# Optimization experiments

Measured on AMD Instinct MI355X. Metric: run time of the kernel, lower is better.

The kernel has to match this reference:

```python
import jax, jax.numpy as jnp
import numpy as np

THRESHOLD = 0.3
NEG_BIG = -2.0 ** 32  # matches tf -2**32 causal mask constant


def setup_inputs() -> dict:
    key = jax.random.key(0)
    kq, kt, kv = jax.random.split(key, 3)
    B, S, D = 16, 2048, 128
    Q = jax.random.normal(kq, (B, S, D), dtype=jnp.float32)
    T = jax.random.normal(kt, (B, S, D), dtype=jnp.float32)
    V = jax.random.normal(kv, (B, S, D), dtype=jnp.float32)
    return {"Q": Q, "T": T, "V": V}


def reference(Q, T, V):
    # scores: [B, S, S]
    A = jnp.einsum('bqd,bkd->bqk', Q, T)
    # Faithful to tf.where(A>thr, A, -2**32 * cast(A>thr)):
    # the false branch evaluates to 0 (mask is 0 there), NOT -2**32.
    A = jnp.where(A > THRESHOLD, A, jnp.zeros((), A.dtype))
    S = Q.shape[1]
    causal = jnp.triu(jnp.ones((S, S), dtype=bool), k=1)  # strictly upper = masked
    A = A + jnp.where(causal, jnp.asarray(NEG_BIG, A.dtype), jnp.zeros((), A.dtype))
    d_k = jnp.asarray(Q.shape[-1], A.dtype)
    A = A / jnp.sqrt(d_k)
    y = jax.nn.softmax(A, axis=-1)
    return jnp.einsum('bqk,bkd->bqd', y, V)
```

## Files before the change

### kernel.cpp

```cpp
#include <hip/hip_runtime.h>
#include <hip/hip_bf16.h>


#define S_LEN 2048
#define D_DIM 128
#define BQ 64
#define BK 64
#define THRESH 0.3f
#define SCALE 0.08838834764831845f

typedef __bf16 bf16x8 __attribute__((ext_vector_type(8)));
typedef float f32x4 __attribute__((ext_vector_type(4)));

__global__ void vt_kernel(const float* __restrict__ V, __bf16* __restrict__ Vt) {
    __shared__ float tile[64][65];
    int bid = blockIdx.x;
    int b  = bid >> 6;
    int t2 = bid & 63;
    int s0 = (t2 >> 1) * 64;
    int d0 = (t2 & 1) * 64;
    int tid = threadIdx.x;
    #pragma unroll
    for (int it = 0; it < 2; ++it) {
        int row = it * 32 + (tid >> 3);
        int c   = (tid & 7) * 8;
        const float* p = V + ((size_t)b * S_LEN + s0 + row) * D_DIM + d0 + c;
        *(f32x4*)(&tile[row][c])     = *(const f32x4*)p;
        *(f32x4*)(&tile[row][c + 4]) = *(const f32x4*)(p + 4);
    }
    __syncthreads();
    #pragma unroll
    for (int it = 0; it < 2; ++it) {
        int dr = it * 32 + (tid >> 3);
        int c  = (tid & 7) * 8;
        bf16x8 w;
        #pragma unroll
        for (int j = 0; j < 8; ++j) w[j] = (__bf16)tile[c + j][dr];
        *(bf16x8*)(Vt + ((size_t)b * D_DIM + d0 + dr) * S_LEN + s0 + c) = w;
    }
}

__global__ __launch_bounds__(512, 2)
void fa_kernel(const float* __restrict__ Q, const float* __restrict__ T,
               const __bf16* __restrict__ Vt, float* __restrict__ O) {
    __shared__ __align__(16) unsigned char smem[81920];

    const int bid = blockIdx.x;
    const int b   = bid & 15;
    const int pi  = bid >> 4;
    const int qtH = 31 - pi;
    const int L   = pi + 1;

    const int tid   = threadIdx.x;
    const int g     = tid >> 8;
    const int tid_g = tid & 255;
    const int lane  = tid & 63;
    const int wg    = tid >> 6;
    const int wv    = wg & 3;
    const int col   = lane & 15;
    const int quad  = lane >> 4;

    unsigned char* Tt = smem + g * 16384;
    unsigned char* Vl = smem + 32768 + g * 16384;
    unsigned char* Pw = smem + 65536 + wg * 2048;

    bf16x8 qf[4];
    auto loadQ = [&](int qt) {
        const float* qptr = Q + ((size_t)b * S_LEN + qt * BQ + wv * 16 + col) * D_DIM + quad * 8;
        #pragma unroll
        for (int kk = 0; kk < 4; ++kk) {
            f32x4 a = *(const f32x4*)(qptr + kk * 32);
            f32x4 c = *(const f32x4*)(qptr + kk * 32 + 4);
            #pragma unroll
            for (int j = 0; j < 4; ++j) { qf[kk][j] = (__bf16)a[j]; qf[kk][4 + j] = (__bf16)c[j]; }
        }
    };

    f32x4 oacc[8];
    float lsum[4];
    auto resetAcc = [&]() {
        #pragma unroll
        for (int dt = 0; dt < 8; ++dt) oacc[dt] = {0.f, 0.f, 0.f, 0.f};
        #pragma unroll
        for (int r = 0; r < 4; ++r) lsum[r] = 0.f;
    };

    f32x4 tr[8]; bf16x8 vr[4];
    auto loadTiles = [&](int k0) {
        #pragma unroll
        for (int it = 0; it < 4; ++it) {
            int flat = it * 2048 + tid_g * 8;
            int row = flat >> 7, c = flat & 127;
            const float* p = T + ((size_t)b * S_LEN + k0 + row) * D_DIM + c;
            tr[2 * it]     = *(const f32x4*)p;
            tr[2 * it + 1] = *(const f32x4*)(p + 4);
        }
        #pragma unroll
        for (int it = 0; it < 4; ++it) {
            int flat = it * 2048 + tid_g * 8;
            int d = flat >> 6, kk2 = flat & 63;
            vr[it] = *(const bf16x8*)(Vt + ((size_t)b * D_DIM + d) * S_LEN + k0 + kk2);
        }
    };
    auto storeTiles = [&]() {
        #pragma unroll
        for (int it = 0; it < 4; ++it) {
            int flat = it * 2048 + tid_g * 8;
            int row = flat >> 7, c = flat & 127;
            bf16x8 w;
            #pragma unroll
            for (int j = 0; j < 4; ++j) {
                w[j]     = (__bf16)tr[2 * it][j];
                w[4 + j] = (__bf16)tr[2 * it + 1][j];
            }
            *(bf16x8*)(Tt + row * 256 + ((c * 2) ^ ((row & 7) << 4))) = w;
        }
        #pragma unroll
        for (int it = 0; it < 4; ++it) {
            int flat = it * 2048 + tid_g * 8;
            int d = flat >> 6, kk2 = flat & 63;
            *(bf16x8*)(Vl + d * 128 + ((kk2 * 2) ^ ((d & 7) << 4))) = vr[it];
        }
    };

    auto computeTile = [&](bool diag) {
        f32x4 sacc[4];
        #pragma unroll
        for (int t = 0; t < 4; ++t) {
            sacc[t] = {0.f, 0.f, 0.f, 0.f};
            #pragma unroll
            for (int kk = 0; kk < 4; ++kk) {
                int row = t * 16 + col;
                bf16x8 bf = *(const bf16x8*)(Tt + row * 256 + ((kk * 64 + quad * 16) ^ ((row & 7) << 4)));
                sacc[t] = __builtin_amdgcn_mfma_f32_16x16x32_bf16(qf[kk], bf, sacc[t], 0, 0, 0);
            }
        }
        float p[4][4];
        #pragma unroll
        for (int t = 0; t < 4; ++t)
            #pragma unroll
            for (int r = 0; r < 4; ++r) {
                float s = sacc[t][r];
                float e = __expf(s * SCALE);
                float w = (s > THRESH) ? e : 1.0f;
                if (diag && (t * 16 + col > wv * 16 + quad * 4 + r)) w = 0.0f;
                p[t][r] = w;
            }
        #pragma unroll
        for (int r = 0; r < 4; ++r)
            lsum[r] += (p[0][r] + p[1][r]) + (p[2][r] + p[3][r]);

        #pragma unroll
        for (int t = 0; t < 4; ++t)
            #pragma unroll
            for (int r = 0; r < 4; ++r) {
                int row = quad * 4 + r;
                *(__bf16*)(Pw + row * 128 + (((t * 16 + col) * 2) ^ ((row & 7) << 4))) = (__bf16)p[t][r];
            }
        asm volatile("s_waitcnt lgkmcnt(0)" ::: "memory");

        #pragma unroll
        for (int ks = 0; ks < 2; ++ks) {
            bf16x8 af = *(const bf16x8*)(Pw + col * 128 + ((ks * 64 + quad * 16) ^ ((col & 7) << 4)));
            #pragma unroll
            for (int dt = 0; dt < 8; ++dt) {
                int row = dt * 16 + col;
                bf16x8 bf = *(const bf16x8*)(Vl + row * 128 + ((ks * 64 + quad * 16) ^ ((row & 7) << 4)));
                oacc[dt] = __builtin_amdgcn_mfma_f32_16x16x32_bf16(af, bf, oacc[dt], 0, 0, 0);
            }
        }
    };

    auto slotKT = [&](int s) -> int {
        if (s >= 17) return -1;
        if (g == 0) return s;
        if (s < L)  return s;
        if (s == L) return -1;
        return s + 15 - pi;
    };

    resetAcc();
    int qtile = (g == 0) ? qtH : pi;
    loadQ(qtile);

    loadTiles(0);
    storeTiles();
    __syncthreads();

    for (int s = 0; s < 17; ++s) {
        int kt  = slotKT(s);
        int ktn = slotKT(s + 1);
        if (ktn >= 0) loadTiles(ktn * BK);
        if (kt >= 0) {
            computeTile(kt == qtile);
        } else {
            float inv[4];
            #pragma unroll
            for (int r = 0; r < 4; ++r) {
                float l = lsum[r];
                l += __shfl_xor(l, 1); l += __shfl_xor(l, 2);
                l += __shfl_xor(l, 4); l += __shfl_xor(l, 8);
                inv[r] = 1.0f / l;
            }
            float* optr = O + ((size_t)b * S_LEN + (size_t)pi * BQ + wv * 16) * D_DIM;
            #pragma unroll
            for (int dt = 0; dt < 8; ++dt)
                #pragma unroll
                for (int r = 0; r < 4; ++r)
                    optr[(quad * 4 + r) * D_DIM + dt * 16 + col] = oacc[dt][r] * inv[r];
            resetAcc();
            qtile = qtH;
            loadQ(qtH);
        }
        __syncthreads();
        if (ktn >= 0) storeTiles();
        __syncthreads();
    }

    float lred[4];
    #pragma unroll
    for (int r = 0; r < 4; ++r) {
        float l = lsum[r];
        l += __shfl_xor(l, 1); l += __shfl_xor(l, 2);
        l += __shfl_xor(l, 4); l += __shfl_xor(l, 8);
        lred[r] = l;
    }

    if (g == 1) {
        #pragma unroll
        for (int dt = 0; dt < 8; ++dt)
            #pragma unroll
            for (int r = 0; r < 4; ++r) {
                int row = wv * 16 + quad * 4 + r;
                *(float*)(smem + row * 512 + (((dt * 16 + col) * 4) ^ ((row & 7) << 4))) = oacc[dt][r];
            }
        if (col == 0) {
            #pragma unroll
            for (int r = 0; r < 4; ++r)
                *(float*)(smem + 65536 + (wv * 16 + quad * 4 + r) * 4) = lred[r];
        }
    }
    __syncthreads();
    if (g == 0) {
        float inv[4];
        #pragma unroll
        for (int r = 0; r < 4; ++r) {
            int row = wv * 16 + quad * 4 + r;
            float lp = *(const float*)(smem + 65536 + row * 4);
            inv[r] = 1.0f / (lred[r] + lp);
        }
        float* optr = O + ((size_t)b * S_LEN + (size_t)qtH * BQ + wv * 16) * D_DIM;
        #pragma unroll
        for (int dt = 0; dt < 8; ++dt)
            #pragma unroll
            for (int r = 0; r < 4; ++r) {
                int row = wv * 16 + quad * 4 + r;
                float part = *(const float*)(smem + row * 512 + (((dt * 16 + col) * 4) ^ ((row & 7) << 4)));
                optr[(quad * 4 + r) * D_DIM + dt * 16 + col] = (oacc[dt][r] + part) * inv[r];
            }
    }
}

extern "C" void kernel_launch(void* const* d_in, const int* in_sizes, int n_in,
                              void* d_out, int out_size, void* d_ws, size_t ws_size,
                              hipStream_t stream) {
    const float* Q = (const float*)d_in[0];
    const float* T = (const float*)d_in[1];
    const float* V = (const float*)d_in[2];
    __bf16* Vt = (__bf16*)d_ws;
    float* O   = (float*)d_out;

    vt_kernel<<<16 * 64, 256, 0, stream>>>(V, Vt);
    fa_kernel<<<16 * 16, 512, 0, stream>>>(Q, T, Vt, O);
}
```

Before: 135.3 us.

## Split KV range across four blocks per pair with global partial-sum reduction

Replaces the 512-thread block, which ran two query tiles in separate halves, with 256-thread blocks. Each block handles one of four KV chunks for a paired (short, long) query-tile set, giving four times as many blocks. Partial outputs and row sums go to workspace, and the last block to arrive, chosen by atomic ticket counters, waits on a done counter, reduces the partials and writes the output. This aims to raise occupancy and balance work across CUs, at the cost of extra global traffic, atomics and a spin-wait that relies on co-residency. It also switches __expf to exp2f with a folded constant.

```diff
diff --git a/kernel.cpp b/kernel.cpp
--- a/kernel.cpp
+++ b/kernel.cpp
@@ -7,19 +7,24 @@
 #define BQ 64
 #define BK 64
 #define THRESH 0.3f
-#define SCALE 0.08838834764831845f
+#define EXP2C 0.12751742f
 
 typedef __bf16 bf16x8 __attribute__((ext_vector_type(8)));
 typedef float f32x4 __attribute__((ext_vector_type(4)));
 
-__global__ void vt_kernel(const float* __restrict__ V, __bf16* __restrict__ Vt) {
+__global__ void vt_kernel(const float* __restrict__ V, __bf16* __restrict__ Vt,
+                          int* __restrict__ ctrs) {
     __shared__ float tile[64][65];
     int bid = blockIdx.x;
+    int tid = threadIdx.x;
+    if (bid == 0) {
+        #pragma unroll
+        for (int i = 0; i < 4; ++i) ctrs[tid * 4 + i] = 0;
+    }
     int b  = bid >> 6;
     int t2 = bid & 63;
     int s0 = (t2 >> 1) * 64;
     int d0 = (t2 & 1) * 64;
-    int tid = threadIdx.x;
     #pragma unroll
     for (int it = 0; it < 2; ++it) {
         int row = it * 32 + (tid >> 3);
@@ -40,29 +45,30 @@
     }
 }
 
-__global__ __launch_bounds__(512, 2)
+__global__ __launch_bounds__(256, 4)
 void fa_kernel(const float* __restrict__ Q, const float* __restrict__ T,
-               const __bf16* __restrict__ Vt, float* __restrict__ O) {
-    __shared__ __align__(16) unsigned char smem[81920];
+               const __bf16* __restrict__ Vt, float* __restrict__ O,
+               float* __restrict__ pO, float* __restrict__ pL,
+               int* __restrict__ cnt, int* __restrict__ done) {
+    __shared__ __align__(16) unsigned char smem[40960];
 
     const int bid = blockIdx.x;
     const int b   = bid & 15;
-    const int pi  = bid >> 4;
+    const int pi  = (bid >> 4) & 15;
+    const int c   = bid >> 8;
     const int qtH = 31 - pi;
     const int L   = pi + 1;
 
-    const int tid   = threadIdx.x;
-    const int g     = tid >> 8;
-    const int tid_g = tid & 255;
-    const int lane  = tid & 63;
-    const int wg    = tid >> 6;
-    const int wv    = wg & 3;
-    const int col   = lane & 15;
-    const int quad  = lane >> 4;
-
-    unsigned char* Tt = smem + g * 16384;
-    unsigned char* Vl = smem + 32768 + g * 16384;
-    unsigned char* Pw = smem + 65536 + wg * 2048;
+    const int tid  = threadIdx.x;
+    const int lane = tid & 63;
+    const int wv   = tid >> 6;
+    const int col  = lane & 15;
+    const int quad = lane >> 4;
+
+    unsigned char* Tt = smem;
+    unsigned char* Vl = smem + 16384;
+    unsigned char* Pw = smem + 32768 + wv * 2048;
+    int* tkp = (int*)(smem + 32768);
 
     bf16x8 qf[4];
     auto loadQ = [&](int qt) {
@@ -70,9 +76,9 @@
         #pragma unroll
         for (int kk = 0; kk < 4; ++kk) {
             f32x4 a = *(const f32x4*)(qptr + kk * 32);
-            f32x4 c = *(const f32x4*)(qptr + kk * 32 + 4);
-            #pragma unroll
-            for (int j = 0; j < 4; ++j) { qf[kk][j] = (__bf16)a[j]; qf[kk][4 + j] = (__bf16)c[j]; }
+            f32x4 d = *(const f32x4*)(qptr + kk * 32 + 4);
+            #pragma unroll
+            for (int j = 0; j < 4; ++j) { qf[kk][j] = (__bf16)a[j]; qf[kk][4 + j] = (__bf16)d[j]; }
         }
     };
 
@@ -89,15 +95,15 @@
     auto loadTiles = [&](int k0) {
         #pragma unroll
         for (int it = 0; it < 4; ++it) {
-            int flat = it * 2048 + tid_g * 8;
-            int row = flat >> 7, c = flat & 127;
-            const float* p = T + ((size_t)b * S_LEN + k0 + row) * D_DIM + c;
+            int flat = it * 2048 + tid * 8;
+            int row = flat >> 7, cc = flat & 127;
+            const float* p = T + ((size_t)b * S_LEN + k0 + row) * D_DIM + cc;
             tr[2 * it]     = *(const f32x4*)p;
             tr[2 * it + 1] = *(const f32x4*)(p + 4);
         }
         #pragma unroll
         for (int it = 0; it < 4; ++it) {
-            int flat = it * 2048 + tid_g * 8;
+            int flat = it * 2048 + tid * 8;
             int d = flat >> 6, kk2 = flat & 63;
             vr[it] = *(const bf16x8*)(Vt + ((size_t)b * D_DIM + d) * S_LEN + k0 + kk2);
         }
@@ -105,19 +111,19 @@
     auto storeTiles = [&]() {
         #pragma unroll
         for (int it = 0; it < 4; ++it) {
-            int flat = it * 2048 + tid_g * 8;
-            int row = flat >> 7, c = flat & 127;
+            int flat = it * 2048 + tid * 8;
+            int row = flat >> 7, cc = flat & 127;
             bf16x8 w;
             #pragma unroll
             for (int j = 0; j < 4; ++j) {
                 w[j]     = (__bf16)tr[2 * it][j];
                 w[4 + j] = (__bf16)tr[2 * it + 1][j];
             }
-            *(bf16x8*)(Tt + row * 256 + ((c * 2) ^ ((row & 7) << 4))) = w;
+            *(bf16x8*)(Tt + row * 256 + ((cc * 2) ^ ((row & 7) << 4))) = w;
         }
         #pragma unroll
         for (int it = 0; it < 4; ++it) {
-            int flat = it * 2048 + tid_g * 8;
+            int flat = it * 2048 + tid * 8;
             int d = flat >> 6, kk2 = flat & 63;
             *(bf16x8*)(Vl + d * 128 + ((kk2 * 2) ^ ((d & 7) << 4))) = vr[it];
         }
@@ -141,7 +147,7 @@
             #pragma unroll
             for (int r = 0; r < 4; ++r) {
                 float s = sacc[t][r];
-                float e = __expf(s * SCALE);
+                float e = exp2f(s * EXP2C);
                 float w = (s > THRESH) ? e : 1.0f;
                 if (diag && (t * 16 + col > wv * 16 + quad * 4 + r)) w = 0.0f;
                 p[t][r] = w;
@@ -171,93 +177,107 @@
         }
     };
 
-    auto slotKT = [&](int s) -> int {
-        if (s >= 17) return -1;
-        if (g == 0) return s;
-        if (s < L)  return s;
-        if (s == L) return -1;
-        return s + 15 - pi;
-    };
-
-    resetAcc();
-    int qtile = (g == 0) ? qtH : pi;
-    loadQ(qtile);
-
-    loadTiles(0);
-    storeTiles();
-    __syncthreads();
-
-    for (int s = 0; s < 17; ++s) {
-        int kt  = slotKT(s);
-        int ktn = slotKT(s + 1);
-        if (ktn >= 0) loadTiles(ktn * BK);
-        if (kt >= 0) {
-            computeTile(kt == qtile);
-        } else {
+    auto runSeg = [&](int qt, int k0t, int nt) {
+        loadQ(qt); resetAcc();
+        loadTiles(k0t * BK);
+        storeTiles();
+        __syncthreads();
+        for (int s = 0; s < nt; ++s) {
+            if (s + 1 < nt) loadTiles((k0t + s + 1) * BK);
+            computeTile(k0t + s == qt);
+            __syncthreads();
+            if (s + 1 < nt) { storeTiles(); __syncthreads(); }
+        }
+    };
+
+    auto storeO = [&](int qt, const float inv[4]) {
+        float* optr = O + ((size_t)b * S_LEN + qt * BQ + wv * 16) * D_DIM;
+        #pragma unroll
+        for (int dt = 0; dt < 8; ++dt)
+            #pragma unroll
+            for (int r = 0; r < 4; ++r)
+                optr[(quad * 4 + r) * D_DIM + dt * 16 + col] = oacc[dt][r] * inv[r];
+    };
+
+    auto flushTarget = [&](int qt, int tgt, int n) {
+        float lred[4];
+        #pragma unroll
+        for (int r = 0; r < 4; ++r) {
+            float l = lsum[r];
+            l += __shfl_xor(l, 1); l += __shfl_xor(l, 2);
+            l += __shfl_xor(l, 4); l += __shfl_xor(l, 8);
+            lred[r] = l;
+        }
+        if (n == 1) {
             float inv[4];
             #pragma unroll
-            for (int r = 0; r < 4; ++r) {
-                float l = lsum[r];
-                l += __shfl_xor(l, 1); l += __shfl_xor(l, 2);
-                l += __shfl_xor(l, 4); l += __shfl_xor(l, 8);
-                inv[r] = 1.0f / l;
-            }
-            float* optr = O + ((size_t)b * S_LEN + (size_t)pi * BQ + wv * 16) * D_DIM;
+            for (int r = 0; r < 4; ++r) inv[r] = 1.0f / lred[r];
+            storeO(qt, inv);
+            return;
+        }
+        const int pairid = b * 16 + pi;
+        const int cidx   = pairid * 2 + tgt;
+        __syncthreads();
+        if (tid == 0)
+            *tkp = __hip_atomic_fetch_add(&cnt[cidx], 1, __ATOMIC_RELAXED, __HIP_MEMORY_SCOPE_AGENT);
+        __syncthreads();
+        int t = *tkp;
+        __syncthreads();
+        if (t < n - 1) {
+            int slot = (tgt == 0) ? 3 : t;
+            float* po = pO + ((size_t)pairid * 4 + slot) * (64 * 128);
+            float* pl = pL + ((size_t)pairid * 4 + slot) * 64;
             #pragma unroll
             for (int dt = 0; dt < 8; ++dt)
                 #pragma unroll
                 for (int r = 0; r < 4; ++r)
-                    optr[(quad * 4 + r) * D_DIM + dt * 16 + col] = oacc[dt][r] * inv[r];
-            resetAcc();
-            qtile = qtH;
-            loadQ(qtH);
-        }
-        __syncthreads();
-        if (ktn >= 0) storeTiles();
-        __syncthreads();
-    }
-
-    float lred[4];
-    #pragma unroll
-    for (int r = 0; r < 4; ++r) {
-        float l = lsum[r];
-        l += __shfl_xor(l, 1); l += __shfl_xor(l, 2);
-        l += __shfl_xor(l, 4); l += __shfl_xor(l, 8);
-        lred[r] = l;
-    }
-
-    if (g == 1) {
-        #pragma unroll
-        for (int dt = 0; dt < 8; ++dt)
-            #pragma unroll
-            for (int r = 0; r < 4; ++r) {
-                int row = wv * 16 + quad * 4 + r;
-                *(float*)(smem + row * 512 + (((dt * 16 + col) * 4) ^ ((row & 7) << 4))) = oacc[dt][r];
-            }
-        if (col == 0) {
-            #pragma unroll
-            for (int r = 0; r < 4; ++r)
-                *(float*)(smem + 65536 + (wv * 16 + quad * 4 + r) * 4) = lred[r];
-        }
-    }
-    __syncthreads();
-    if (g == 0) {
-        float inv[4];
-        #pragma unroll
-        for (int r = 0; r < 4; ++r) {
-            int row = wv * 16 + quad * 4 + r;
-            float lp = *(const float*)(smem + 65536 + row * 4);
-            inv[r] = 1.0f / (lred[r] + lp);
-        }
-        float* optr = O + ((size_t)b * S_LEN + (size_t)qtH * BQ + wv * 16) * D_DIM;
-        #pragma unroll
-        for (int dt = 0; dt < 8; ++dt)
-            #pragma unroll
-            for (int r = 0; r < 4; ++r) {
-                int row = wv * 16 + quad * 4 + r;
-                float part = *(const float*)(smem + row * 512 + (((dt * 16 + col) * 4) ^ ((row & 7) << 4)));
-                optr[(quad * 4 + r) * D_DIM + dt * 16 + col] = (oacc[dt][r] + part) * inv[r];
-            }
+                    po[(wv * 16 + quad * 4 + r) * 128 + dt * 16 + col] = oacc[dt][r];
+            if (col == 0) {
+                #pragma unroll
+                for (int r = 0; r < 4; ++r) pl[wv * 16 + quad * 4 + r] = lred[r];
+            }
+            __threadfence();
+            __syncthreads();
+            if (tid == 0)
+                __hip_atomic_fetch_add(&done[cidx], 1, __ATOMIC_RELEASE, __HIP_MEMORY_SCOPE_AGENT);
+        } else {
+            if (tid == 0) {
+                while (__hip_atomic_load(&done[cidx], __ATOMIC_ACQUIRE, __HIP_MEMORY_SCOPE_AGENT) < n - 1)
+                    __builtin_amdgcn_s_sleep(8);
+            }
+            __syncthreads();
+            __threadfence();
+            for (int s = 0; s < n - 1; ++s) {
+                int slot = (tgt == 0) ? 3 : s;
+                const float* po = pO + ((size_t)pairid * 4 + slot) * (64 * 128);
+                const float* pl = pL + ((size_t)pairid * 4 + slot) * 64;
+                #pragma unroll
+                for (int dt = 0; dt < 8; ++dt)
+                    #pragma unroll
+                    for (int r = 0; r < 4; ++r)
+                        oacc[dt][r] += po[(wv * 16 + quad * 4 + r) * 128 + dt * 16 + col];
+                #pragma unroll
+                for (int r = 0; r < 4; ++r) lred[r] += pl[wv * 16 + quad * 4 + r];
+            }
+            float inv[4];
+            #pragma unroll
+            for (int r = 0; r < 4; ++r) inv[r] = 1.0f / lred[r];
+            storeO(qt, inv);
+        }
+    };
+
+    const int Btab[5] = {0, 9, 17, 25, 33};
+    const int lo = Btab[c], hi = Btab[c + 1];
+
+    int lend = L < hi ? L : hi;
+    if (lo < lend) {
+        runSeg(pi, lo, lend - lo);
+        flushTarget(pi, 0, 1 + (L >= 10));
+    }
+    int hstart = L > lo ? L : lo;
+    if (hstart < hi) {
+        runSeg(qtH, hstart - L, hi - hstart);
+        flushTarget(qtH, 1, 4 - (L >= 9));
     }
 }
 
@@ -267,9 +287,16 @@
     const float* Q = (const float*)d_in[0];
     const float* T = (const float*)d_in[1];
     const float* V = (const float*)d_in[2];
-    __bf16* Vt = (__bf16*)d_ws;
-    float* O   = (float*)d_out;
-
-    vt_kernel<<<16 * 64, 256, 0, stream>>>(V, Vt);
-    fa_kernel<<<16 * 16, 512, 0, stream>>>(Q, T, Vt, O);
+    float* O = (float*)d_out;
+
+    unsigned char* ws = (unsigned char*)d_ws;
+    __bf16* Vt = (__bf16*)ws;
+    float* pO  = (float*)(ws + 8388608);
+    float* pL  = (float*)(ws + 8388608 + 33554432);
+    int*  ctrs = (int*)(ws + 8388608 + 33554432 + 262144);
+    int*  cnt  = ctrs;
+    int*  done = ctrs + 512;
+
+    vt_kernel<<<16 * 64, 256, 0, stream>>>(V, Vt, ctrs);
+    fa_kernel<<<16 * 16 * 4, 256, 0, stream>>>(Q, T, Vt, O, pO, pL, cnt, done);
 }
```

After: 445.0 us. +228.9%, slower.
